# Performance work log

Measured on AMD Instinct MI355X. Metric: run time of the kernel, lower is better.

The kernel has to match this reference:

```python
import jax, jax.numpy as jnp
import numpy as np


def setup_inputs() -> dict:
    key = jax.random.key(0)
    k1, k2, k3 = jax.random.split(key, 3)
    C_in, C_out, K = 64, 64, 3
    x = jax.random.normal(k1, (32, C_in, 128, 128), dtype=jnp.float32)
    # Conv2d default init scale: U(-b, b) with b = 1/sqrt(fan_in)
    bound = 1.0 / np.sqrt(C_in * K * K)
    conv_weight = jax.random.uniform(k2, (C_out, C_in, K, K), dtype=jnp.float32,
                                     minval=-bound, maxval=bound)
    conv_bias = jax.random.uniform(k3, (C_out,), dtype=jnp.float32,
                                   minval=-bound, maxval=bound)
    return {"x": x, "conv_weight": conv_weight, "conv_bias": conv_bias}


def reference(x, conv_weight, conv_bias):
    # Conv2d, stride=1, padding=0 (VALID), NCHW/OIHW
    y = jax.lax.conv_general_dilated(
        x, conv_weight,
        window_strides=(1, 1), padding="VALID",
        dimension_numbers=("NCHW", "OIHW", "NCHW"),
    ) + conv_bias[None, :, None, None]
    # min over output channels (keepdim) then double tanh
    m = jnp.min(y, axis=1, keepdims=True)  # (N, 1, OH, OW)
    return jnp.tanh(jnp.tanh(m))
```

## Files before the change

kernel.cpp:

```cpp
#include <hip/hip_runtime.h>
#include <hip/hip_bf16.h>

typedef __attribute__((ext_vector_type(8))) short        short8;
typedef __attribute__((ext_vector_type(8))) __bf16       bf16x8;
typedef __attribute__((ext_vector_type(4))) float        f32x4;
typedef __attribute__((ext_vector_type(4))) unsigned int u32x4;

#define NB 32
#define CI 64
#define H  128
#define W  128
#define OH 126
#define OW 126
#define HW (H*W)

#define TCOLS 66
#define RSTRIDE 80
#define LDS_BYTES (6*TCOLS*RSTRIDE)

__device__ __forceinline__ unsigned int f2bf(float f) {
    unsigned int u = __builtin_bit_cast(unsigned int, f);
    u += 0x7fffu + ((u >> 16) & 1u);
    return u >> 16;
}

__device__ __forceinline__ unsigned int cvt_pk(float lo, float hi) {
    unsigned int r;
    asm("v_cvt_pk_bf16_f32 %0, %1, %2" : "=v"(r) : "v"(lo), "v"(hi));
    return r;
}

__device__ __forceinline__ float fast_tanh(float x) {
    float e = __builtin_amdgcn_exp2f(x * 2.8853900817779268f);
    float r = __builtin_amdgcn_rcpf(e + 1.0f);
    return 1.0f - 2.0f * r;
}

__global__ void wxform(const float* __restrict__ w, unsigned short* __restrict__ ws) {
    int tid = blockIdx.x * 256 + threadIdx.x;
    if (tid >= 18*4*64*8) return;
    int j   = tid & 7;
    int l   = (tid >> 3) & 63;
    int cf  = (tid >> 9) & 3;
    int ks  = tid >> 11;
    int co  = cf*16 + (l & 15);
    int ci  = (ks & 1)*32 + ((l >> 4) << 3) + j;
    int khw = ks >> 1;
    int kh  = khw / 3, kw = khw % 3;
    float v = w[co*(CI*9) + ci*9 + kh*3 + kw];
    ws[tid] = (unsigned short)f2bf(v);
}

__global__ __launch_bounds__(256, 4)
void conv_min_tanh(const float* __restrict__ x,
                   const unsigned short* __restrict__ wfrag,
                   const float* __restrict__ bias,
                   float* __restrict__ out) {
    __shared__ __align__(16) char xs[LDS_BYTES];

    const int lane = threadIdx.x & 63;
    const int wv   = threadIdx.x >> 6;
    const int c0   = blockIdx.x * 64;
    const int r0   = blockIdx.y * 4;
    const int b    = blockIdx.z;
    const float* xb = x + (size_t)b * CI * HW;

    const int lane_c = lane & 15;
    const int hi     = lane >> 4;

    const short8* wp = (const short8*)wfrag;
    const int orow = r0 + wv;
    const bool live = (orow < OH);

    f32x4 acc[4][4];
    #pragma unroll
    for (int m = 0; m < 4; ++m)
        #pragma unroll
        for (int cf = 0; cf < 4; ++cf)
            acc[m][cf] = (f32x4){0.f, 0.f, 0.f, 0.f};

    const int abase = (wv*TCOLS + lane_c)*RSTRIDE + hi*16;

    #pragma unroll
    for (int cih = 0; cih < 2; ++cih) {
        #pragma unroll
        for (int i = 0; i < 6; ++i) {
            const int tsk = wv + 4*i;
            const int r   = tsk >> 2;
            const int p   = tsk & 3;
            const int gr  = r0 + r;
            float f0=0.f,f1=0.f,f2=0.f,f3=0.f,f4=0.f,f5=0.f,f6=0.f,f7=0.f;
            if (gr < H) {
                const float* xp = xb + (size_t)(cih*32 + p*8)*HW + gr*W + c0 + lane;
                f0 = xp[0];    f1 = xp[HW];   f2 = xp[2*HW]; f3 = xp[3*HW];
                f4 = xp[4*HW]; f5 = xp[5*HW]; f6 = xp[6*HW]; f7 = xp[7*HW];
            }
            u32x4 pk;
            pk.x = cvt_pk(f0, f1); pk.y = cvt_pk(f2, f3);
            pk.z = cvt_pk(f4, f5); pk.w = cvt_pk(f6, f7);
            *(u32x4*)(xs + (r*TCOLS + lane)*RSTRIDE + p*16) = pk;
        }
        if (threadIdx.x < 48) {
            const int r  = threadIdx.x >> 3;
            const int cc = (threadIdx.x >> 2) & 1;
            const int p  = threadIdx.x & 3;
            const int gr = r0 + r;
            const int gc = c0 + 64 + cc;
            float f0=0.f,f1=0.f,f2=0.f,f3=0.f,f4=0.f,f5=0.f,f6=0.f,f7=0.f;
            if (gr < H && gc < W) {
                const float* xq = xb + (size_t)(cih*32 + p*8)*HW + gr*W + gc;
                f0 = xq[0];    f1 = xq[HW];   f2 = xq[2*HW]; f3 = xq[3*HW];
                f4 = xq[4*HW]; f5 = xq[5*HW]; f6 = xq[6*HW]; f7 = xq[7*HW];
            }
            u32x4 pk;
            pk.x = cvt_pk(f0, f1); pk.y = cvt_pk(f2, f3);
            pk.z = cvt_pk(f4, f5); pk.w = cvt_pk(f6, f7);
            *(u32x4*)(xs + (r*TCOLS + 64 + cc)*RSTRIDE + p*16) = pk;
        }
        __syncthreads();

        if (live) {
            #pragma unroll
            for (int khw = 0; khw < 9; ++khw) {
                short8 wfb[4];
                #pragma unroll
                for (int cf = 0; cf < 4; ++cf)
                    wfb[cf] = wp[((khw*2 + cih)*4 + cf)*64 + lane];
                const int kh = khw/3, kw = khw%3;
                #pragma unroll
                for (int m = 0; m < 4; ++m) {
                    const short8 av = *(const short8*)(
                        xs + abase + (kh*TCOLS + kw + m*16)*RSTRIDE);
                    const bf16x8 a = __builtin_bit_cast(bf16x8, av);
                    #pragma unroll
                    for (int cf = 0; cf < 4; ++cf)
                        acc[m][cf] = __builtin_amdgcn_mfma_f32_16x16x32_bf16(
                            a, __builtin_bit_cast(bf16x8, wfb[cf]), acc[m][cf], 0, 0, 0);
                }
            }
        }
        if (cih == 0) __syncthreads();
    }

    if (!live) return;

    const float bs0 = bias[lane_c], bs1 = bias[16 + lane_c],
                bs2 = bias[32 + lane_c], bs3 = bias[48 + lane_c];
    float* outp = out + (b*OH + orow)*OW;
    #pragma unroll
    for (int m = 0; m < 4; ++m) {
        #pragma unroll
        for (int rg = 0; rg < 4; ++rg) {
            float v0 = fminf(fminf(acc[m][0][rg] + bs0, acc[m][1][rg] + bs1),
                             fminf(acc[m][2][rg] + bs2, acc[m][3][rg] + bs3));
            v0 = fminf(v0, __shfl_xor(v0, 1));
            v0 = fminf(v0, __shfl_xor(v0, 2));
            v0 = fminf(v0, __shfl_xor(v0, 4));
            v0 = fminf(v0, __shfl_xor(v0, 8));
            const float vt = fast_tanh(fast_tanh(v0));
            const int ocol = c0 + m*16 + hi*4 + rg;
            if (lane_c == 0 && ocol < OW) outp[ocol] = vt;
        }
    }
}

extern "C" void kernel_launch(void* const* d_in, const int* in_sizes, int n_in,
                              void* d_out, int out_size, void* d_ws, size_t ws_size,
                              hipStream_t stream) {
    const float* x    = (const float*)d_in[0];
    const float* w    = (const float*)d_in[1];
    const float* bias = (const float*)d_in[2];
    float* out        = (float*)d_out;
    unsigned short* wbuf = (unsigned short*)d_ws;

    wxform<<<dim3(144), dim3(256), 0, stream>>>(w, wbuf);
    conv_min_tanh<<<dim3(2, 32, NB), dim3(256), 0, stream>>>(x, wbuf, bias, out);
}
```

Measured before the change: 73.01 us.

## Stage all 64 input channels once and split columns across 8 waves

The block grows to 512 threads, and all 64 input channels are staged into LDS in a single pass with a wider row stride, which removes the second staging phase and its extra barriers. Each wave now computes half of an output row (2 column fragments instead of 4), which doubles wave-level parallelism per block. Weight fragments are double-buffered in registers across the 18 K-steps. The cost is a larger LDS footprint per block, which may lower the number of resident blocks, and the stride of 144 may change the LDS bank conflict pattern.

```diff
diff --git a/kernel.cpp b/kernel.cpp
--- a/kernel.cpp
+++ b/kernel.cpp
@@ -15,7 +15,7 @@
 #define HW (H*W)
 
 #define TCOLS 66
-#define RSTRIDE 80
+#define RSTRIDE 144
 #define LDS_BYTES (6*TCOLS*RSTRIDE)
 
 __device__ __forceinline__ unsigned int f2bf(float f) {
@@ -51,7 +51,7 @@
     ws[tid] = (unsigned short)f2bf(v);
 }
 
-__global__ __launch_bounds__(256, 4)
+__global__ __launch_bounds__(512, 4)
 void conv_min_tanh(const float* __restrict__ x,
                    const unsigned short* __restrict__ wfrag,
                    const float* __restrict__ bias,
@@ -68,87 +68,91 @@
     const int lane_c = lane & 15;
     const int hi     = lane >> 4;
 
+    #pragma unroll
+    for (int i = 0; i < 6; ++i) {
+        const int task = wv + 8*i;
+        const int r    = task >> 3;
+        const int q    = task & 7;
+        const int gr   = r0 + r;
+        float f0=0.f,f1=0.f,f2=0.f,f3=0.f,f4=0.f,f5=0.f,f6=0.f,f7=0.f;
+        if (gr < H) {
+            const float* xp = xb + (size_t)(q*8)*HW + gr*W + c0 + lane;
+            f0 = xp[0];    f1 = xp[HW];   f2 = xp[2*HW]; f3 = xp[3*HW];
+            f4 = xp[4*HW]; f5 = xp[5*HW]; f6 = xp[6*HW]; f7 = xp[7*HW];
+        }
+        u32x4 pk;
+        pk.x = cvt_pk(f0, f1); pk.y = cvt_pk(f2, f3);
+        pk.z = cvt_pk(f4, f5); pk.w = cvt_pk(f6, f7);
+        *(u32x4*)(xs + (r*TCOLS + lane)*RSTRIDE + q*16) = pk;
+    }
+    if (threadIdx.x < 96) {
+        const int r  = threadIdx.x >> 4;
+        const int sub = threadIdx.x & 15;
+        const int cc = sub >> 3;
+        const int q  = sub & 7;
+        const int gr = r0 + r;
+        const int gc = c0 + 64 + cc;
+        float f0=0.f,f1=0.f,f2=0.f,f3=0.f,f4=0.f,f5=0.f,f6=0.f,f7=0.f;
+        if (gr < H && gc < W) {
+            const float* xq = xb + (size_t)(q*8)*HW + gr*W + gc;
+            f0 = xq[0];    f1 = xq[HW];   f2 = xq[2*HW]; f3 = xq[3*HW];
+            f4 = xq[4*HW]; f5 = xq[5*HW]; f6 = xq[6*HW]; f7 = xq[7*HW];
+        }
+        u32x4 pk;
+        pk.x = cvt_pk(f0, f1); pk.y = cvt_pk(f2, f3);
+        pk.z = cvt_pk(f4, f5); pk.w = cvt_pk(f6, f7);
+        *(u32x4*)(xs + (r*TCOLS + 64 + cc)*RSTRIDE + q*16) = pk;
+    }
+    __syncthreads();
+
+    const int wr   = wv >> 1;
+    const int ch   = wv & 1;
+    const int orow = r0 + wr;
+    if (orow >= OH) return;
+
     const short8* wp = (const short8*)wfrag;
-    const int orow = r0 + wv;
-    const bool live = (orow < OH);
 
-    f32x4 acc[4][4];
+    f32x4 acc[2][4];
     #pragma unroll
-    for (int m = 0; m < 4; ++m)
+    for (int m = 0; m < 2; ++m)
         #pragma unroll
         for (int cf = 0; cf < 4; ++cf)
             acc[m][cf] = (f32x4){0.f, 0.f, 0.f, 0.f};
 
-    const int abase = (wv*TCOLS + lane_c)*RSTRIDE + hi*16;
+    const int abase = (wr*TCOLS + ch*32 + lane_c)*RSTRIDE + hi*16;
+
+    short8 wfb[2][4];
+    #pragma unroll
+    for (int cf = 0; cf < 4; ++cf)
+        wfb[0][cf] = wp[cf*64 + lane];
 
     #pragma unroll
-    for (int cih = 0; cih < 2; ++cih) {
+    for (int ks = 0; ks < 18; ++ks) {
+        const int buf = ks & 1;
+        if (ks < 17) {
+            #pragma unroll
+            for (int cf = 0; cf < 4; ++cf)
+                wfb[buf^1][cf] = wp[((ks+1)*4 + cf)*64 + lane];
+        }
+        const int khw = ks >> 1, cih = ks & 1;
+        const int kh = khw/3, kw = khw%3;
         #pragma unroll
-        for (int i = 0; i < 6; ++i) {
-            const int tsk = wv + 4*i;
-            const int r   = tsk >> 2;
-            const int p   = tsk & 3;
-            const int gr  = r0 + r;
-            float f0=0.f,f1=0.f,f2=0.f,f3=0.f,f4=0.f,f5=0.f,f6=0.f,f7=0.f;
-            if (gr < H) {
-                const float* xp = xb + (size_t)(cih*32 + p*8)*HW + gr*W + c0 + lane;
-                f0 = xp[0];    f1 = xp[HW];   f2 = xp[2*HW]; f3 = xp[3*HW];
-                f4 = xp[4*HW]; f5 = xp[5*HW]; f6 = xp[6*HW]; f7 = xp[7*HW];
-            }
-            u32x4 pk;
-            pk.x = cvt_pk(f0, f1); pk.y = cvt_pk(f2, f3);
-            pk.z = cvt_pk(f4, f5); pk.w = cvt_pk(f6, f7);
-            *(u32x4*)(xs + (r*TCOLS + lane)*RSTRIDE + p*16) = pk;
+        for (int m = 0; m < 2; ++m) {
+            const short8 av = *(const short8*)(
+                xs + abase + kh*(TCOLS*RSTRIDE) + (kw + m*16)*RSTRIDE + cih*64);
+            const bf16x8 a = __builtin_bit_cast(bf16x8, av);
+            #pragma unroll
+            for (int cf = 0; cf < 4; ++cf)
+                acc[m][cf] = __builtin_amdgcn_mfma_f32_16x16x32_bf16(
+                    a, __builtin_bit_cast(bf16x8, wfb[buf][cf]), acc[m][cf], 0, 0, 0);
         }
-        if (threadIdx.x < 48) {
-            const int r  = threadIdx.x >> 3;
-            const int cc = (threadIdx.x >> 2) & 1;
-            const int p  = threadIdx.x & 3;
-            const int gr = r0 + r;
-            const int gc = c0 + 64 + cc;
-            float f0=0.f,f1=0.f,f2=0.f,f3=0.f,f4=0.f,f5=0.f,f6=0.f,f7=0.f;
-            if (gr < H && gc < W) {
-                const float* xq = xb + (size_t)(cih*32 + p*8)*HW + gr*W + gc;
-                f0 = xq[0];    f1 = xq[HW];   f2 = xq[2*HW]; f3 = xq[3*HW];
-                f4 = xq[4*HW]; f5 = xq[5*HW]; f6 = xq[6*HW]; f7 = xq[7*HW];
-            }
-            u32x4 pk;
-            pk.x = cvt_pk(f0, f1); pk.y = cvt_pk(f2, f3);
-            pk.z = cvt_pk(f4, f5); pk.w = cvt_pk(f6, f7);
-            *(u32x4*)(xs + (r*TCOLS + 64 + cc)*RSTRIDE + p*16) = pk;
-        }
-        __syncthreads();
-
-        if (live) {
-            #pragma unroll
-            for (int khw = 0; khw < 9; ++khw) {
-                short8 wfb[4];
-                #pragma unroll
-                for (int cf = 0; cf < 4; ++cf)
-                    wfb[cf] = wp[((khw*2 + cih)*4 + cf)*64 + lane];
-                const int kh = khw/3, kw = khw%3;
-                #pragma unroll
-                for (int m = 0; m < 4; ++m) {
-                    const short8 av = *(const short8*)(
-                        xs + abase + (kh*TCOLS + kw + m*16)*RSTRIDE);
-                    const bf16x8 a = __builtin_bit_cast(bf16x8, av);
-                    #pragma unroll
-                    for (int cf = 0; cf < 4; ++cf)
-                        acc[m][cf] = __builtin_amdgcn_mfma_f32_16x16x32_bf16(
-                            a, __builtin_bit_cast(bf16x8, wfb[cf]), acc[m][cf], 0, 0, 0);
-                }
-            }
-        }
-        if (cih == 0) __syncthreads();
     }
-
-    if (!live) return;
 
     const float bs0 = bias[lane_c], bs1 = bias[16 + lane_c],
                 bs2 = bias[32 + lane_c], bs3 = bias[48 + lane_c];
     float* outp = out + (b*OH + orow)*OW;
     #pragma unroll
-    for (int m = 0; m < 4; ++m) {
+    for (int m = 0; m < 2; ++m) {
         #pragma unroll
         for (int rg = 0; rg < 4; ++rg) {
             float v0 = fminf(fminf(acc[m][0][rg] + bs0, acc[m][1][rg] + bs1),
@@ -158,7 +162,7 @@
             v0 = fminf(v0, __shfl_xor(v0, 4));
             v0 = fminf(v0, __shfl_xor(v0, 8));
             const float vt = fast_tanh(fast_tanh(v0));
-            const int ocol = c0 + m*16 + hi*4 + rg;
+            const int ocol = c0 + ch*32 + m*16 + hi*4 + rg;
             if (lane_c == 0 && ocol < OW) outp[ocol] = vt;
         }
     }
@@ -174,5 +178,5 @@
     unsigned short* wbuf = (unsigned short*)d_ws;
 
     wxform<<<dim3(144), dim3(256), 0, stream>>>(w, wbuf);
-    conv_min_tanh<<<dim3(2, 32, NB), dim3(256), 0, stream>>>(x, wbuf, bias, out);
+    conv_min_tanh<<<dim3(2, 32, NB), dim3(512), 0, stream>>>(x, wbuf, bias, out);
 }
```

New measurement: 75.49 us. +3.4%, slower.

## Double-buffer LDS channel halves and loop over four images per block

Applied to the files above, without the earlier changes.

The kernel now uses two LDS buffers so that staging the next 32-channel half overlaps MFMA compute on the current half. Each persistent block handles four batch images in turn, and the block grows to 512 threads, with each wave covering half the columns of one output row. The goal is to hide global-load latency behind compute and reduce launch and tail overhead. In exchange the grid has four times fewer blocks, LDS use per block doubles, and the longer sequential chain per block could lower occupancy.

```diff
diff --git a/kernel.cpp b/kernel.cpp
--- a/kernel.cpp
+++ b/kernel.cpp
@@ -16,7 +16,7 @@
 
 #define TCOLS 66
 #define RSTRIDE 80
-#define LDS_BYTES (6*TCOLS*RSTRIDE)
+#define HBYTES (6*TCOLS*RSTRIDE)
 
 __device__ __forceinline__ unsigned int f2bf(float f) {
     unsigned int u = __builtin_bit_cast(unsigned int, f);
@@ -51,116 +51,137 @@
     ws[tid] = (unsigned short)f2bf(v);
 }
 
-__global__ __launch_bounds__(256, 4)
+__device__ __forceinline__ void stage_half(const float* __restrict__ xh,
+                                           char* __restrict__ buf,
+                                           int r0, int c0, int wv, int lane, int tid) {
+    #pragma unroll
+    for (int i = 0; i < 3; ++i) {
+        const int task = wv + 8*i;
+        const int r    = task >> 2;
+        const int p    = task & 3;
+        const int gr   = r0 + r;
+        float f0=0.f,f1=0.f,f2=0.f,f3=0.f,f4=0.f,f5=0.f,f6=0.f,f7=0.f;
+        if (gr < H) {
+            const float* xp = xh + (size_t)(p*8)*HW + gr*W + c0 + lane;
+            f0 = xp[0];    f1 = xp[HW];   f2 = xp[2*HW]; f3 = xp[3*HW];
+            f4 = xp[4*HW]; f5 = xp[5*HW]; f6 = xp[6*HW]; f7 = xp[7*HW];
+        }
+        u32x4 pk;
+        pk.x = cvt_pk(f0, f1); pk.y = cvt_pk(f2, f3);
+        pk.z = cvt_pk(f4, f5); pk.w = cvt_pk(f6, f7);
+        *(u32x4*)(buf + (r*TCOLS + lane)*RSTRIDE + p*16) = pk;
+    }
+    if (tid < 48) {
+        const int r  = tid >> 3;
+        const int cc = (tid >> 2) & 1;
+        const int p  = tid & 3;
+        const int gr = r0 + r;
+        const int gc = c0 + 64 + cc;
+        float f0=0.f,f1=0.f,f2=0.f,f3=0.f,f4=0.f,f5=0.f,f6=0.f,f7=0.f;
+        if (gr < H && gc < W) {
+            const float* xq = xh + (size_t)(p*8)*HW + gr*W + gc;
+            f0 = xq[0];    f1 = xq[HW];   f2 = xq[2*HW]; f3 = xq[3*HW];
+            f4 = xq[4*HW]; f5 = xq[5*HW]; f6 = xq[6*HW]; f7 = xq[7*HW];
+        }
+        u32x4 pk;
+        pk.x = cvt_pk(f0, f1); pk.y = cvt_pk(f2, f3);
+        pk.z = cvt_pk(f4, f5); pk.w = cvt_pk(f6, f7);
+        *(u32x4*)(buf + (r*TCOLS + 64 + cc)*RSTRIDE + p*16) = pk;
+    }
+}
+
+__device__ __forceinline__ void compute_half(const char* __restrict__ buf,
+                                             const short8* __restrict__ wp,
+                                             int cih, int abase, int lane,
+                                             f32x4 acc[2][4]) {
+    #pragma unroll
+    for (int khw = 0; khw < 9; ++khw) {
+        short8 wfb[4];
+        #pragma unroll
+        for (int cf = 0; cf < 4; ++cf)
+            wfb[cf] = wp[((khw*2 + cih)*4 + cf)*64 + lane];
+        const int kh = khw/3, kw = khw%3;
+        #pragma unroll
+        for (int m = 0; m < 2; ++m) {
+            const short8 av = *(const short8*)(
+                buf + abase + (kh*TCOLS + kw + m*16)*RSTRIDE);
+            const bf16x8 a = __builtin_bit_cast(bf16x8, av);
+            #pragma unroll
+            for (int cf = 0; cf < 4; ++cf)
+                acc[m][cf] = __builtin_amdgcn_mfma_f32_16x16x32_bf16(
+                    a, __builtin_bit_cast(bf16x8, wfb[cf]), acc[m][cf], 0, 0, 0);
+        }
+    }
+}
+
+__global__ __launch_bounds__(512, 4)
 void conv_min_tanh(const float* __restrict__ x,
                    const unsigned short* __restrict__ wfrag,
                    const float* __restrict__ bias,
                    float* __restrict__ out) {
-    __shared__ __align__(16) char xs[LDS_BYTES];
+    __shared__ __align__(16) char xs0[HBYTES];
+    __shared__ __align__(16) char xs1[HBYTES];
 
-    const int lane = threadIdx.x & 63;
-    const int wv   = threadIdx.x >> 6;
+    const int tid  = threadIdx.x;
+    const int lane = tid & 63;
+    const int wv   = tid >> 6;
     const int c0   = blockIdx.x * 64;
     const int r0   = blockIdx.y * 4;
-    const int b    = blockIdx.z;
-    const float* xb = x + (size_t)b * CI * HW;
+    const int bz   = blockIdx.z;
 
     const int lane_c = lane & 15;
     const int hi     = lane >> 4;
+    const int wr     = wv >> 1;
+    const int ch     = wv & 1;
+    const int orow   = r0 + wr;
+    const bool live  = (orow < OH);
 
     const short8* wp = (const short8*)wfrag;
-    const int orow = r0 + wv;
-    const bool live = (orow < OH);
+    const int abase  = (wr*TCOLS + ch*32 + lane_c)*RSTRIDE + hi*16;
 
-    f32x4 acc[4][4];
-    #pragma unroll
-    for (int m = 0; m < 4; ++m)
+    const float bs0 = bias[lane_c], bs1 = bias[16 + lane_c],
+                bs2 = bias[32 + lane_c], bs3 = bias[48 + lane_c];
+
+    stage_half(x + (size_t)(bz*4)*CI*HW, xs0, r0, c0, wv, lane, tid);
+    __syncthreads();
+
+    #pragma unroll 1
+    for (int t = 0; t < 4; ++t) {
+        const int b = bz*4 + t;
+        const float* xb = x + (size_t)b*CI*HW;
+
+        f32x4 acc[2][4];
         #pragma unroll
-        for (int cf = 0; cf < 4; ++cf)
-            acc[m][cf] = (f32x4){0.f, 0.f, 0.f, 0.f};
+        for (int m = 0; m < 2; ++m)
+            #pragma unroll
+            for (int cf = 0; cf < 4; ++cf)
+                acc[m][cf] = (f32x4){0.f, 0.f, 0.f, 0.f};
 
-    const int abase = (wv*TCOLS + lane_c)*RSTRIDE + hi*16;
-
-    #pragma unroll
-    for (int cih = 0; cih < 2; ++cih) {
-        #pragma unroll
-        for (int i = 0; i < 6; ++i) {
-            const int tsk = wv + 4*i;
-            const int r   = tsk >> 2;
-            const int p   = tsk & 3;
-            const int gr  = r0 + r;
-            float f0=0.f,f1=0.f,f2=0.f,f3=0.f,f4=0.f,f5=0.f,f6=0.f,f7=0.f;
-            if (gr < H) {
-                const float* xp = xb + (size_t)(cih*32 + p*8)*HW + gr*W + c0 + lane;
-                f0 = xp[0];    f1 = xp[HW];   f2 = xp[2*HW]; f3 = xp[3*HW];
-                f4 = xp[4*HW]; f5 = xp[5*HW]; f6 = xp[6*HW]; f7 = xp[7*HW];
-            }
-            u32x4 pk;
-            pk.x = cvt_pk(f0, f1); pk.y = cvt_pk(f2, f3);
-            pk.z = cvt_pk(f4, f5); pk.w = cvt_pk(f6, f7);
-            *(u32x4*)(xs + (r*TCOLS + lane)*RSTRIDE + p*16) = pk;
-        }
-        if (threadIdx.x < 48) {
-            const int r  = threadIdx.x >> 3;
-            const int cc = (threadIdx.x >> 2) & 1;
-            const int p  = threadIdx.x & 3;
-            const int gr = r0 + r;
-            const int gc = c0 + 64 + cc;
-            float f0=0.f,f1=0.f,f2=0.f,f3=0.f,f4=0.f,f5=0.f,f6=0.f,f7=0.f;
-            if (gr < H && gc < W) {
-                const float* xq = xb + (size_t)(cih*32 + p*8)*HW + gr*W + gc;
-                f0 = xq[0];    f1 = xq[HW];   f2 = xq[2*HW]; f3 = xq[3*HW];
-                f4 = xq[4*HW]; f5 = xq[5*HW]; f6 = xq[6*HW]; f7 = xq[7*HW];
-            }
-            u32x4 pk;
-            pk.x = cvt_pk(f0, f1); pk.y = cvt_pk(f2, f3);
-            pk.z = cvt_pk(f4, f5); pk.w = cvt_pk(f6, f7);
-            *(u32x4*)(xs + (r*TCOLS + 64 + cc)*RSTRIDE + p*16) = pk;
-        }
+        stage_half(xb + (size_t)32*HW, xs1, r0, c0, wv, lane, tid);
+        if (live) compute_half(xs0, wp, 0, abase, lane, acc);
         __syncthreads();
 
+        if (t < 3) stage_half(xb + (size_t)CI*HW, xs0, r0, c0, wv, lane, tid);
         if (live) {
+            compute_half(xs1, wp, 1, abase, lane, acc);
+            float* outp = out + (size_t)(b*OH + orow)*OW;
             #pragma unroll
-            for (int khw = 0; khw < 9; ++khw) {
-                short8 wfb[4];
+            for (int m = 0; m < 2; ++m) {
                 #pragma unroll
-                for (int cf = 0; cf < 4; ++cf)
-                    wfb[cf] = wp[((khw*2 + cih)*4 + cf)*64 + lane];
-                const int kh = khw/3, kw = khw%3;
-                #pragma unroll
-                for (int m = 0; m < 4; ++m) {
-                    const short8 av = *(const short8*)(
-                        xs + abase + (kh*TCOLS + kw + m*16)*RSTRIDE);
-                    const bf16x8 a = __builtin_bit_cast(bf16x8, av);
-                    #pragma unroll
-                    for (int cf = 0; cf < 4; ++cf)
-                        acc[m][cf] = __builtin_amdgcn_mfma_f32_16x16x32_bf16(
-                            a, __builtin_bit_cast(bf16x8, wfb[cf]), acc[m][cf], 0, 0, 0);
+                for (int rg = 0; rg < 4; ++rg) {
+                    float v0 = fminf(fminf(acc[m][0][rg] + bs0, acc[m][1][rg] + bs1),
+                                     fminf(acc[m][2][rg] + bs2, acc[m][3][rg] + bs3));
+                    v0 = fminf(v0, __shfl_xor(v0, 1));
+                    v0 = fminf(v0, __shfl_xor(v0, 2));
+                    v0 = fminf(v0, __shfl_xor(v0, 4));
+                    v0 = fminf(v0, __shfl_xor(v0, 8));
+                    const float vt = fast_tanh(fast_tanh(v0));
+                    const int ocol = c0 + ch*32 + m*16 + hi*4 + rg;
+                    if (lane_c == 0 && ocol < OW) outp[ocol] = vt;
                 }
             }
         }
-        if (cih == 0) __syncthreads();
-    }
-
-    if (!live) return;
-
-    const float bs0 = bias[lane_c], bs1 = bias[16 + lane_c],
-                bs2 = bias[32 + lane_c], bs3 = bias[48 + lane_c];
-    float* outp = out + (b*OH + orow)*OW;
-    #pragma unroll
-    for (int m = 0; m < 4; ++m) {
-        #pragma unroll
-        for (int rg = 0; rg < 4; ++rg) {
-            float v0 = fminf(fminf(acc[m][0][rg] + bs0, acc[m][1][rg] + bs1),
-                             fminf(acc[m][2][rg] + bs2, acc[m][3][rg] + bs3));
-            v0 = fminf(v0, __shfl_xor(v0, 1));
-            v0 = fminf(v0, __shfl_xor(v0, 2));
-            v0 = fminf(v0, __shfl_xor(v0, 4));
-            v0 = fminf(v0, __shfl_xor(v0, 8));
-            const float vt = fast_tanh(fast_tanh(v0));
-            const int ocol = c0 + m*16 + hi*4 + rg;
-            if (lane_c == 0 && ocol < OW) outp[ocol] = vt;
-        }
+        __syncthreads();
     }
 }
 
@@ -174,5 +195,5 @@
     unsigned short* wbuf = (unsigned short*)d_ws;
 
     wxform<<<dim3(144), dim3(256), 0, stream>>>(w, wbuf);
-    conv_min_tanh<<<dim3(2, 32, NB), dim3(256), 0, stream>>>(x, wbuf, bias, out);
+    conv_min_tanh<<<dim3(2, 32, 8), dim3(512), 0, stream>>>(x, wbuf, bias, out);
 }
```

New measurement: 149.3 us. 2.04x slower.
